# Kernel tuning notes

Hardware: AMD Instinct MI355X
Metric: run time of the kernel (lower is better)

## Reference

```python
import jax, jax.numpy as jnp
import numpy as np

EPS = 1e-5


def setup_inputs() -> dict:
    key = jax.random.key(0)
    k_u, k_v, k_w, k_g, k_b, k_m, k_var = jax.random.split(key, 7)
    B, S, C1, C2, H, W = 4, 8, 64, 64, 128, 128
    CC = C1 + C2  # concat channels = out channels = 128
    u = jax.random.normal(k_u, (B, 1, C1, H, W), dtype=jnp.float32)
    v = jax.random.normal(k_v, (B, S, C2, H, W), dtype=jnp.float32)
    conv_w = jax.random.normal(k_w, (CC, CC, 3, 3), dtype=jnp.float32) * 0.05  # OIHW
    bn_gamma = jnp.ones((CC,), jnp.float32) + 0.1 * jax.random.normal(k_g, (CC,), dtype=jnp.float32)
    bn_beta = 0.1 * jax.random.normal(k_b, (CC,), dtype=jnp.float32)
    bn_mean = 0.1 * jax.random.normal(k_m, (CC,), dtype=jnp.float32)
    bn_var = jnp.abs(jax.random.normal(k_var, (CC,), dtype=jnp.float32)) + 0.5
    return {"u": u, "v": v, "conv_w": conv_w, "bn_gamma": bn_gamma,
            "bn_beta": bn_beta, "bn_mean": bn_mean, "bn_var": bn_var}


def _cross_conv(u, v, conv_w, bn_gamma, bn_beta, bn_mean, bn_var):
    B, _, C1, H, W = u.shape
    _, S, C2, _, _ = v.shape
    # broadcast u over the s axis, concat channels -> (b*s, c1+c2, h, w)
    us = jnp.broadcast_to(u[:, 0, None], (B, S, C1, H, W))
    xy = jnp.concatenate([us, v], axis=2).reshape(B * S, C1 + C2, H, W)
    # 3x3 conv, stride 1, SAME padding, no bias (BN follows)
    y = jax.lax.conv_general_dilated(
        xy, conv_w, window_strides=(1, 1), padding=((1, 1), (1, 1)),
        dimension_numbers=("NCHW", "OIHW", "NCHW"))
    # BatchNorm (inference: running stats)
    scale = (bn_gamma * jax.lax.rsqrt(bn_var + EPS))[None, :, None, None]
    shift = (bn_beta - bn_mean * bn_gamma * jax.lax.rsqrt(bn_var + EPS))[None, :, None, None]
    y = y * scale + shift
    # skip = Identity (concat_channels == out_channels, stride 1), then ReLU
    out = jax.nn.relu(y + xy)
    return out.reshape(B, 1, S, C1 + C2, H, W)


def reference(u, v, conv_w, bn_gamma, bn_beta, bn_mean, bn_var):
    return _cross_conv(u, v, conv_w, bn_gamma, bn_beta, bn_mean, bn_var)
```

## Files before the change

### kernel.cpp

```cpp
#include <hip/hip_runtime.h>
#include <hip/hip_bf16.h>


#define EPS 1e-5f

typedef __attribute__((ext_vector_type(8))) short short8;
typedef __attribute__((ext_vector_type(4))) float f32x4;

constexpr int C1 = 64, CC = 128, Hd = 128, Wd = 128;
constexpr int HW = Hd * Wd;
constexpr int SP = 18;
constexpr int ROW = 40;
constexpr int WFRAGS = 9 * 4 * 8;

__global__ void prep_weights(const float* __restrict__ wgt, ushort* __restrict__ wf) {
    int idx = blockIdx.x * 256 + threadIdx.x;
    if (idx >= WFRAGS * 64) return;
    int l  = idx & 63;
    int f  = idx >> 6;
    int cf = f & 7;
    int c  = (f >> 3) & 3;
    int t  = f >> 5;
    int kh = t / 3, kw = t % 3;
    int co  = cf * 16 + (l & 15);
    int cib = c * 32 + (l >> 4) * 8;
    ushort* dst = wf + (size_t)idx * 8;
#pragma unroll
    for (int j = 0; j < 8; ++j) {
        float x = wgt[(((size_t)co * CC + cib + j) * 3 + kh) * 3 + kw];
        __hip_bfloat16 b = __float2bfloat16(x);
        dst[j] = *(ushort*)&b;
    }
}

__global__ __launch_bounds__(256, 2)
void crossconv_mfma(const float* __restrict__ u,
                    const float* __restrict__ v,
                    const ushort* __restrict__ wf,
                    const float* __restrict__ gamma,
                    const float* __restrict__ beta,
                    const float* __restrict__ mean,
                    const float* __restrict__ var,
                    float* __restrict__ out) {
    __shared__ ushort in_s[SP * SP * ROW];
    __shared__ float s_sc[CC], s_sh[CC];

    const int tid = threadIdx.x;
    const int w0 = blockIdx.x * 16;
    const int h0 = blockIdx.y * 16;
    const int n  = blockIdx.z;
    const int b  = n >> 3;
    const float* __restrict__ ubase = u + (size_t)b * C1 * HW;
    const float* __restrict__ vbase = v + (size_t)n * C1 * HW;

    if (tid < CC) {
        float sc = gamma[tid] * rsqrtf(var[tid] + EPS);
        s_sc[tid] = sc;
        s_sh[tid] = beta[tid] - mean[tid] * sc;
    }

    const int l    = tid & 63;
    const int wid  = tid >> 6;
    const int n16  = l & 15;
    const int kgrp = l >> 4;

    f32x4 acc[8][4];
#pragma unroll
    for (int cf = 0; cf < 8; ++cf)
#pragma unroll
        for (int pf = 0; pf < 4; ++pf) acc[cf][pf] = (f32x4)0.f;

    for (int c = 0; c < 4; ++c) {
        __syncthreads();
        for (int e = tid; e < 32 * SP * SP; e += 256) {
            int ci_l = e / (SP * SP);
            int r    = e - ci_l * (SP * SP);
            int sph  = r / SP;
            int spw  = r - sph * SP;
            int gh = h0 + sph - 1, gw = w0 + spw - 1;
            int ci = c * 32 + ci_l;
            float val = 0.f;
            if ((unsigned)gh < (unsigned)Hd && (unsigned)gw < (unsigned)Wd) {
                const float* base = (ci < C1) ? (ubase + (size_t)ci * HW)
                                              : (vbase + (size_t)(ci - C1) * HW);
                val = base[gh * Wd + gw];
            }
            __hip_bfloat16 bv = __float2bfloat16(val);
            in_s[(sph * SP + spw) * ROW + ci_l] = *(ushort*)&bv;
        }
        __syncthreads();

#pragma unroll
        for (int t = 0; t < 9; ++t) {
            const int kh = t / 3, kw = t % 3;
            short8 bfr[4];
#pragma unroll
            for (int pf = 0; pf < 4; ++pf) {
                int sph = wid * 4 + pf + kh;
                int spw = n16 + kw;
                bfr[pf] = *(const short8*)&in_s[(sph * SP + spw) * ROW + kgrp * 8];
            }
            const short8* wp = (const short8*)wf + ((size_t)(t * 4 + c) * 8) * 64 + l;
#pragma unroll
            for (int cf = 0; cf < 8; ++cf) {
                short8 afr = wp[(size_t)cf * 64];
#pragma unroll
                for (int pf = 0; pf < 4; ++pf)
                    acc[cf][pf] = __builtin_amdgcn_mfma_f32_16x16x32_bf16(
                        afr, bfr[pf], acc[cf][pf], 0, 0, 0);
            }
        }
    }

#pragma unroll
    for (int cf = 0; cf < 8; ++cf) {
#pragma unroll
        for (int pf = 0; pf < 4; ++pf) {
            const int h = h0 + wid * 4 + pf;
            const int w = w0 + n16;
#pragma unroll
            for (int r = 0; r < 4; ++r) {
                const int co = cf * 16 + kgrp * 4 + r;
                const float* base = (co < C1) ? (ubase + (size_t)co * HW)
                                              : (vbase + (size_t)(co - C1) * HW);
                const float x = base[h * Wd + w];
                const float y = fmaf(acc[cf][pf][r], s_sc[co], s_sh[co]) + x;
                out[((size_t)n * CC + co) * HW + h * Wd + w] = fmaxf(y, 0.f);
            }
        }
    }
}

extern "C" void kernel_launch(void* const* d_in, const int* in_sizes, int n_in,
                              void* d_out, int out_size, void* d_ws, size_t ws_size,
                              hipStream_t stream) {
    const float* u     = (const float*)d_in[0];
    const float* v     = (const float*)d_in[1];
    const float* wgt   = (const float*)d_in[2];
    const float* gamma = (const float*)d_in[3];
    const float* beta  = (const float*)d_in[4];
    const float* mean  = (const float*)d_in[5];
    const float* var   = (const float*)d_in[6];
    float* out = (float*)d_out;
    ushort* wf = (ushort*)d_ws;

    prep_weights<<<dim3((WFRAGS * 64 + 255) / 256), dim3(256), 0, stream>>>(wgt, wf);
    crossconv_mfma<<<dim3(Wd / 16, Hd / 16, 32), dim3(256), 0, stream>>>(
        u, v, wf, gamma, beta, mean, var, out);
}
```

Measured before the change: 873.3 us.

## Reuse u-channel conv partials across S and double-buffer shared input staging

Each block now handles one batch element across all 8 S slices. It computes the conv contribution of the shared u channels once and copies that partial accumulator as the starting point for every v slice, so the u half of the convolution is no longer recomputed eight times. Input staging is double-buffered with register prefetch of float2 pairs, and the MFMA operands are swapped so the epilogue can do vectorized float4 loads and stores. The trade-offs are a grid 8x smaller (256 blocks of 512 threads), a serial chain of 18 chunks per block, and higher register pressure.

Result: slower. 977.4 us (+11.9%).

```diff
diff --git a/kernel.cpp b/kernel.cpp
--- a/kernel.cpp
+++ b/kernel.cpp
@@ -6,12 +6,17 @@
 
 typedef __attribute__((ext_vector_type(8))) short short8;
 typedef __attribute__((ext_vector_type(4))) float f32x4;
+typedef __attribute__((ext_vector_type(2))) float f32x2;
 
 constexpr int C1 = 64, CC = 128, Hd = 128, Wd = 128;
 constexpr int HW = Hd * Wd;
 constexpr int SP = 18;
 constexpr int ROW = 40;
 constexpr int WFRAGS = 9 * 4 * 8;
+constexpr int NCHUNK = 18;
+constexpr int UNITS = 16 * 18 * 10;
+constexpr int NTHR = 512;
+constexpr int NU = (UNITS + NTHR - 1) / NTHR;
 
 __global__ void prep_weights(const float* __restrict__ wgt, ushort* __restrict__ wf) {
     int idx = blockIdx.x * 256 + threadIdx.x;
@@ -28,12 +33,12 @@
 #pragma unroll
     for (int j = 0; j < 8; ++j) {
         float x = wgt[(((size_t)co * CC + cib + j) * 3 + kh) * 3 + kw];
-        __hip_bfloat16 b = __float2bfloat16(x);
-        dst[j] = *(ushort*)&b;
+        __hip_bfloat16 bb = __float2bfloat16(x);
+        dst[j] = *(ushort*)&bb;
     }
 }
 
-__global__ __launch_bounds__(256, 2)
+__global__ __launch_bounds__(NTHR, 2)
 void crossconv_mfma(const float* __restrict__ u,
                     const float* __restrict__ v,
                     const ushort* __restrict__ wf,
@@ -42,92 +47,148 @@
                     const float* __restrict__ mean,
                     const float* __restrict__ var,
                     float* __restrict__ out) {
-    __shared__ ushort in_s[SP * SP * ROW];
+    __shared__ alignas(16) ushort in_s[2][SP * SP * ROW];
     __shared__ float s_sc[CC], s_sh[CC];
 
     const int tid = threadIdx.x;
     const int w0 = blockIdx.x * 16;
     const int h0 = blockIdx.y * 16;
-    const int n  = blockIdx.z;
-    const int b  = n >> 3;
+    const int b  = blockIdx.z;
     const float* __restrict__ ubase = u + (size_t)b * C1 * HW;
-    const float* __restrict__ vbase = v + (size_t)n * C1 * HW;
+    const float* __restrict__ vbase = v + (size_t)b * 8 * C1 * HW;
 
     if (tid < CC) {
         float sc = gamma[tid] * rsqrtf(var[tid] + EPS);
         s_sc[tid] = sc;
         s_sh[tid] = beta[tid] - mean[tid] * sc;
     }
-
-    const int l    = tid & 63;
-    const int wid  = tid >> 6;
-    const int n16  = l & 15;
-    const int kgrp = l >> 4;
-
-    f32x4 acc[8][4];
-#pragma unroll
-    for (int cf = 0; cf < 8; ++cf)
-#pragma unroll
-        for (int pf = 0; pf < 4; ++pf) acc[cf][pf] = (f32x4)0.f;
-
-    for (int c = 0; c < 4; ++c) {
-        __syncthreads();
-        for (int e = tid; e < 32 * SP * SP; e += 256) {
-            int ci_l = e / (SP * SP);
-            int r    = e - ci_l * (SP * SP);
-            int sph  = r / SP;
-            int spw  = r - sph * SP;
-            int gh = h0 + sph - 1, gw = w0 + spw - 1;
-            int ci = c * 32 + ci_l;
-            float val = 0.f;
-            if ((unsigned)gh < (unsigned)Hd && (unsigned)gw < (unsigned)Wd) {
-                const float* base = (ci < C1) ? (ubase + (size_t)ci * HW)
-                                              : (vbase + (size_t)(ci - C1) * HW);
-                val = base[gh * Wd + gw];
-            }
-            __hip_bfloat16 bv = __float2bfloat16(val);
-            in_s[(sph * SP + spw) * ROW + ci_l] = *(ushort*)&bv;
-        }
-        __syncthreads();
-
+    {
+        uint4 z{0u, 0u, 0u, 0u};
+        uint4* p = (uint4*)&in_s[0][0];
+        for (int i = tid; i < 2 * SP * SP * ROW / 8; i += NTHR) p[i] = z;
+    }
+
+    const int l = tid & 63, wid = tid >> 6;
+    const int n16 = l & 15, kgrp = l >> 4;
+
+    f32x4 accU[8][2], accV[8][2];
+#pragma unroll
+    for (int cf = 0; cf < 8; ++cf) {
+        accU[cf][0] = (f32x4)0.f; accU[cf][1] = (f32x4)0.f;
+    }
+
+    f32x2 sa[NU], sb[NU];
+    int   sidx[NU];
+    uint  sm0 = 0, sm1 = 0;
+
+    auto chunk_src = [&](int k) -> const float* {
+        if (k < 2) return ubase + (size_t)k * 32 * HW;
+        int km = k - 2;
+        return vbase + ((size_t)(km >> 1) * C1 + (size_t)(km & 1) * 32) * HW;
+    };
+
+    auto stage_load = [&](const float* __restrict__ src) {
+        sm0 = sm1 = 0;
+#pragma unroll
+        for (int i = 0; i < NU; ++i) {
+            int e = tid + i * NTHR;
+            sa[i] = f32x2{0.f, 0.f}; sb[i] = f32x2{0.f, 0.f}; sidx[i] = 0;
+            if (e < UNITS) {
+                int cp  = e / 180;
+                int r   = e - cp * 180;
+                int sph = r / 10;
+                int j   = r - sph * 10;
+                int gh  = h0 + sph - 1;
+                int gw  = w0 + 2 * j - 2;
+                sidx[i] = (sph * SP + 2 * j) * ROW + 2 * cp;
+                if ((unsigned)gh < (unsigned)Hd && (unsigned)gw < (unsigned)(Wd - 1)) {
+                    const float* p = src + (size_t)(2 * cp) * HW + gh * Wd + gw;
+                    sa[i] = *(const f32x2*)p;
+                    sb[i] = *(const f32x2*)(p + HW);
+                    if (j >= 1) sm0 |= 1u << i;
+                    if (j <= 8) sm1 |= 1u << i;
+                }
+            }
+        }
+    };
+
+    auto stage_write = [&](int buf) {
+        ushort* __restrict__ d = in_s[buf];
+#pragma unroll
+        for (int i = 0; i < NU; ++i) {
+            __hip_bfloat16 ax = __float2bfloat16(sa[i].x);
+            __hip_bfloat16 bx = __float2bfloat16(sb[i].x);
+            __hip_bfloat16 ay = __float2bfloat16(sa[i].y);
+            __hip_bfloat16 by = __float2bfloat16(sb[i].y);
+            uint v0 = (uint)*(ushort*)&ax | ((uint)*(ushort*)&bx << 16);
+            uint v1 = (uint)*(ushort*)&ay | ((uint)*(ushort*)&by << 16);
+            if (sm0 & (1u << i)) *(uint*)&d[sidx[i] - ROW] = v0;
+            if (sm1 & (1u << i)) *(uint*)&d[sidx[i]]       = v1;
+        }
+    };
+
+    auto compute = [&](int buf, int c, f32x4 (&acc)[8][2]) {
+        const ushort* __restrict__ bs = in_s[buf];
 #pragma unroll
         for (int t = 0; t < 9; ++t) {
             const int kh = t / 3, kw = t % 3;
-            short8 bfr[4];
-#pragma unroll
-            for (int pf = 0; pf < 4; ++pf) {
-                int sph = wid * 4 + pf + kh;
-                int spw = n16 + kw;
-                bfr[pf] = *(const short8*)&in_s[(sph * SP + spw) * ROW + kgrp * 8];
-            }
-            const short8* wp = (const short8*)wf + ((size_t)(t * 4 + c) * 8) * 64 + l;
+            const int spw = n16 + kw;
+            short8 p0 = *(const short8*)&bs[((wid * 2 + 0 + kh) * SP + spw) * ROW + kgrp * 8];
+            short8 p1 = *(const short8*)&bs[((wid * 2 + 1 + kh) * SP + spw) * ROW + kgrp * 8];
+            const short8* __restrict__ wp =
+                (const short8*)wf + ((size_t)(t * 4 + c) * 8) * 64 + l;
 #pragma unroll
             for (int cf = 0; cf < 8; ++cf) {
-                short8 afr = wp[(size_t)cf * 64];
-#pragma unroll
-                for (int pf = 0; pf < 4; ++pf)
-                    acc[cf][pf] = __builtin_amdgcn_mfma_f32_16x16x32_bf16(
-                        afr, bfr[pf], acc[cf][pf], 0, 0, 0);
-            }
-        }
-    }
-
-#pragma unroll
-    for (int cf = 0; cf < 8; ++cf) {
-#pragma unroll
-        for (int pf = 0; pf < 4; ++pf) {
-            const int h = h0 + wid * 4 + pf;
-            const int w = w0 + n16;
-#pragma unroll
-            for (int r = 0; r < 4; ++r) {
-                const int co = cf * 16 + kgrp * 4 + r;
-                const float* base = (co < C1) ? (ubase + (size_t)co * HW)
-                                              : (vbase + (size_t)(co - C1) * HW);
-                const float x = base[h * Wd + w];
-                const float y = fmaf(acc[cf][pf][r], s_sc[co], s_sh[co]) + x;
-                out[((size_t)n * CC + co) * HW + h * Wd + w] = fmaxf(y, 0.f);
-            }
-        }
+                short8 wfr = wp[(size_t)cf * 64];
+                acc[cf][0] = __builtin_amdgcn_mfma_f32_16x16x32_bf16(p0, wfr, acc[cf][0], 0, 0, 0);
+                acc[cf][1] = __builtin_amdgcn_mfma_f32_16x16x32_bf16(p1, wfr, acc[cf][1], 0, 0, 0);
+            }
+        }
+    };
+
+    __syncthreads();
+    stage_load(chunk_src(0));
+    stage_write(0);
+    __syncthreads();
+
+    for (int k = 0; k < NCHUNK; ++k) {
+        const int cur = k & 1;
+        if (k + 1 < NCHUNK) stage_load(chunk_src(k + 1));
+        if (k >= 2 && (k & 1) == 0) {
+#pragma unroll
+            for (int cf = 0; cf < 8; ++cf) {
+                accV[cf][0] = accU[cf][0]; accV[cf][1] = accU[cf][1];
+            }
+        }
+        const int c = (k < 2) ? k : 2 + ((k - 2) & 1);
+        if (k < 2) compute(cur, c, accU);
+        else       compute(cur, c, accV);
+        if (k + 1 < NCHUNK) stage_write(cur ^ 1);
+        if (k >= 3 && (k & 1)) {
+            const int s = (k - 3) >> 1;
+            const size_t n = (size_t)b * 8 + s;
+#pragma unroll
+            for (int cf = 0; cf < 8; ++cf) {
+                const int co = cf * 16 + n16;
+                const float sc = s_sc[co], sh = s_sh[co];
+                const float* __restrict__ xb = (cf < 4)
+                    ? (ubase + (size_t)co * HW)
+                    : (vbase + ((size_t)s * C1 + (co - C1)) * HW);
+                float* __restrict__ ob = out + ((size_t)n * CC + co) * HW;
+#pragma unroll
+                for (int pf = 0; pf < 2; ++pf) {
+                    const int off = (h0 + wid * 2 + pf) * Wd + w0 + kgrp * 4;
+                    f32x4 x = *(const f32x4*)(xb + off);
+                    f32x4 a = accV[cf][pf];
+                    f32x4 y;
+#pragma unroll
+                    for (int r = 0; r < 4; ++r)
+                        y[r] = fmaxf(fmaf(a[r], sc, sh) + x[r], 0.f);
+                    *(f32x4*)(ob + off) = y;
+                }
+            }
+        }
+        __syncthreads();
     }
 }
 
@@ -145,6 +206,6 @@
     ushort* wf = (ushort*)d_ws;
 
     prep_weights<<<dim3((WFRAGS * 64 + 255) / 256), dim3(256), 0, stream>>>(wgt, wf);
-    crossconv_mfma<<<dim3(Wd / 16, Hd / 16, 32), dim3(256), 0, stream>>>(
+    crossconv_mfma<<<dim3(Wd / 16, Hd / 16, 4), dim3(NTHR), 0, stream>>>(
         u, v, wf, gamma, beta, mean, var, out);
 }
```
